# Kernel optimization log

Hardware: AMD Instinct MI355X
Metric: run time of the kernel (lower is better)

The kernel has to match this reference:

```python
import jax, jax.numpy as jnp
import numpy as np

HEADS = 8
DIM_HEAD = 64


def setup_inputs() -> dict:
    key = jax.random.key(0)
    ks = jax.random.split(key, 9)
    b, n, d = 2, 2048, 512
    inner = HEADS * DIM_HEAD  # 512
    s = 0.02
    return {
        "x": jax.random.normal(ks[0], (b, n, d), dtype=jnp.float32),
        "attn_bias": jax.random.normal(ks[1], (1, HEADS, n, n), dtype=jnp.float32),
        "Wq": jax.random.normal(ks[2], (d, inner), dtype=jnp.float32) * s,
        "Wkv": jax.random.normal(ks[3], (d, 2 * inner), dtype=jnp.float32) * s,
        "Wo": jax.random.normal(ks[4], (inner, d), dtype=jnp.float32) * s,
        "bo": jax.random.normal(ks[5], (d,), dtype=jnp.float32) * s,
        "Wg": jax.random.normal(ks[6], (d, inner), dtype=jnp.float32) * s,
        "bg": jnp.ones((inner,), dtype=jnp.float32),
    }


def reference(x, attn_bias, Wq, Wkv, Wo, bo, Wg, bg):
    b, n, d = x.shape
    h, dh = HEADS, DIM_HEAD
    scale = dh ** -0.5
    # projections: [b, n, h*dh] -> [b, h, n, dh]
    q = (x @ Wq).reshape(b, n, h, dh).transpose(0, 2, 1, 3) * scale
    k, v = jnp.split(x @ Wkv, 2, axis=-1)
    k = k.reshape(b, n, h, dh).transpose(0, 2, 1, 3)
    v = v.reshape(b, n, h, dh).transpose(0, 2, 1, 3)
    # scores + additive bias; max-subtract softmax (stable, as in original)
    dots = jnp.einsum('bhid,bhjd->bhij', q, k) + attn_bias
    attn = jax.nn.softmax(dots, axis=-1)
    out = jnp.einsum('bhij,bhjd->bhid', attn, v)
    out = out.transpose(0, 2, 1, 3).reshape(b, n, h * dh)
    # gating sigmoid epilogue
    gates = jax.nn.sigmoid(x @ Wg + bg)
    out = out * gates
    return out @ Wo + bo
```

## Files before the change

kernel.cpp:

```cpp
#include <hip/hip_runtime.h>
#include <hip/hip_bf16.h>

typedef __bf16 bf16_t;
typedef __bf16 bf16x8 __attribute__((ext_vector_type(8)));
typedef __bf16 bf16x4 __attribute__((ext_vector_type(4)));
typedef short short4v __attribute__((ext_vector_type(4)));
typedef float f32x4 __attribute__((ext_vector_type(4)));

static __device__ __forceinline__ bf16_t to_bf16(float f) { return (bf16_t)f; }

static __device__ __forceinline__ f32x4 mfma16x16x16bf16(bf16x4 a, bf16x4 b, f32x4 c) {
#if __has_builtin(__builtin_amdgcn_mfma_f32_16x16x16bf16_1k)
  return __builtin_amdgcn_mfma_f32_16x16x16bf16_1k(
      *reinterpret_cast<short4v*>(&a), *reinterpret_cast<short4v*>(&b), c, 0, 0, 0);
#else
  f32x4 d;
  asm volatile("v_mfma_f32_16x16x16_bf16 %0, %1, %2, %3"
               : "=v"(d) : "v"(a), "v"(b), "v"(c));
  return d;
#endif
}

__global__ void k_convert_x(const float* __restrict__ src, bf16_t* __restrict__ dst, int n8) {
  int i = blockIdx.x * blockDim.x + threadIdx.x;
  if (i >= n8) return;
  const float4* s = reinterpret_cast<const float4*>(src) + (size_t)i * 2;
  float4 a = s[0], b = s[1];
  bf16x8 v;
  v[0]=(bf16_t)a.x; v[1]=(bf16_t)a.y; v[2]=(bf16_t)a.z; v[3]=(bf16_t)a.w;
  v[4]=(bf16_t)b.x; v[5]=(bf16_t)b.y; v[6]=(bf16_t)b.z; v[7]=(bf16_t)b.w;
  reinterpret_cast<bf16x8*>(dst)[i] = v;
}

__global__ void k_transpose_cvt(const float* __restrict__ src, bf16_t* __restrict__ dst, int Nc) {
  __shared__ bf16_t tile[64 * 72];
  const int n0 = blockIdx.x * 64, k0 = blockIdx.y * 64;
  const int t = threadIdx.x;
  #pragma unroll
  for (int it = 0; it < 16; ++it) {
    int c = t + it * 256;
    int kl = c >> 6, nl = c & 63;
    tile[kl * 72 + nl] = to_bf16(src[(size_t)(k0 + kl) * Nc + n0 + nl]);
  }
  __syncthreads();
  #pragma unroll
  for (int it = 0; it < 16; ++it) {
    int c = t + it * 256;
    int nl = c >> 6, kl = c & 63;
    dst[(size_t)(n0 + nl) * 512 + k0 + kl] = tile[kl * 72 + nl];
  }
}

__global__ __launch_bounds__(256) void k_gemm_proj(
    const bf16_t* __restrict__ A,
    const bf16_t* __restrict__ BT,
    const float*  __restrict__ bg,
    bf16_t* __restrict__ qo,
    bf16_t* __restrict__ ko,
    bf16_t* __restrict__ vto,
    float*  __restrict__ go)
{
  __shared__ __align__(16) bf16_t lA[128 * 72];
  __shared__ __align__(16) bf16_t lB[128 * 72];
  const int t = threadIdx.x;
  const int w = t >> 6, lane = t & 63, lr = lane & 15, lg = lane >> 4;
  const int wr = w >> 1, wc = w & 1;
  const int m0 = blockIdx.y * 128, n0 = blockIdx.x * 128;
  f32x4 acc[4][4] = {};
  for (int k0 = 0; k0 < 512; k0 += 64) {
    __syncthreads();
    #pragma unroll
    for (int it = 0; it < 4; ++it) {
      int c = t + it * 256;
      int row = c >> 3, cc = c & 7;
      *reinterpret_cast<bf16x8*>(&lA[row * 72 + cc * 8]) =
          *reinterpret_cast<const bf16x8*>(&A[(size_t)(m0 + row) * 512 + k0 + cc * 8]);
      *reinterpret_cast<bf16x8*>(&lB[row * 72 + cc * 8]) =
          *reinterpret_cast<const bf16x8*>(&BT[(size_t)(n0 + row) * 512 + k0 + cc * 8]);
    }
    __syncthreads();
    #pragma unroll
    for (int kk = 0; kk < 2; ++kk) {
      bf16x8 af[4], bfm[4];
      #pragma unroll
      for (int mf = 0; mf < 4; ++mf)
        af[mf] = *reinterpret_cast<const bf16x8*>(&lA[(wr*64 + mf*16 + lr) * 72 + kk*32 + lg*8]);
      #pragma unroll
      for (int nf = 0; nf < 4; ++nf)
        bfm[nf] = *reinterpret_cast<const bf16x8*>(&lB[(wc*64 + nf*16 + lr) * 72 + kk*32 + lg*8]);
      #pragma unroll
      for (int mf = 0; mf < 4; ++mf)
        #pragma unroll
        for (int nf = 0; nf < 4; ++nf)
          acc[mf][nf] = __builtin_amdgcn_mfma_f32_16x16x32_bf16(af[mf], bfm[nf], acc[mf][nf], 0, 0, 0);
    }
  }
  const int seg = n0 >> 9;
  #pragma unroll
  for (int mf = 0; mf < 4; ++mf) {
    #pragma unroll
    for (int nf = 0; nf < 4; ++nf) {
      #pragma unroll
      for (int r = 0; r < 4; ++r) {
        int rm = m0 + wr*64 + mf*16 + lg*4 + r;
        int cn = n0 + wc*64 + nf*16 + lr;
        float v = acc[mf][nf][r];
        int b = rm >> 11, n = rm & 2047;
        int c = cn & 511;
        if (seg == 0) {
          int h = c >> 6, dh = c & 63;
          qo[((size_t)(b*8 + h) * 2048 + n) * 64 + dh] = to_bf16(v * 0.125f);
        } else if (seg == 1) {
          int h = c >> 6, dh = c & 63;
          ko[((size_t)(b*8 + h) * 2048 + n) * 64 + dh] = to_bf16(v);
        } else if (seg == 2) {
          int h = c >> 6, dh = c & 63;
          vto[((size_t)(b*8 + h) * 64 + dh) * 2048 + n] = to_bf16(v);
        } else {
          float z = v + bg[c];
          go[(size_t)rm * 512 + c] = 1.0f / (1.0f + __expf(-z));
        }
      }
    }
  }
}

#define M_FIX 8.0f
template<int FINAL>
__global__ __launch_bounds__(256, 4) void k_attn(
    const bf16_t* __restrict__ q,
    const bf16_t* __restrict__ kb,
    const bf16_t* __restrict__ vt,
    const float*  __restrict__ bias,
    const float*  __restrict__ gates,
    bf16_t* __restrict__ ao,
    float* __restrict__ pO,
    float* __restrict__ pl)
{
  __shared__ __align__(16) bf16_t lK[64 * 72];
  __shared__ __align__(16) bf16_t lV[64 * 72];
  const int t = threadIdx.x, w = t >> 6, lane = t & 63, lr = lane & 15, lg = lane >> 4;
  const int bh = blockIdx.y, b = bh >> 3, h = bh & 7;
  const int i0 = blockIdx.x * 64, ib = i0 + w * 16;
  const int ntile = 32 / (int)gridDim.z;
  const int sz = blockIdx.z;
  const int jbase = sz * ntile * 64;

  bf16x8 aq[2];
  const bf16_t* qp = q + ((size_t)bh * 2048 + ib + lr) * 64;
  aq[0] = *reinterpret_cast<const bf16x8*>(qp + lg * 8);
  aq[1] = *reinterpret_cast<const bf16x8*>(qp + 32 + lg * 8);

  float l_lane = 0.f;
  f32x4 accO[4] = {};

  const float* bias_p = bias + (size_t)h * 2048 * 2048 + (size_t)(ib + lr) * 2048 + lg * 4;
  const bf16_t* kp = kb + (size_t)bh * 2048 * 64;
  const bf16_t* vp = vt + (size_t)bh * 64 * 2048;

  const int srow = t >> 3, scc = t & 7;
  const int srow1 = (t + 256) >> 3;

  bf16x8 rK0, rK1, rV0, rV1;
  float4 bv4[4];
  {
    const int j0 = jbase;
    rK0 = *reinterpret_cast<const bf16x8*>(&kp[(size_t)(j0 + srow)  * 64 + scc * 8]);
    rK1 = *reinterpret_cast<const bf16x8*>(&kp[(size_t)(j0 + srow1) * 64 + scc * 8]);
    rV0 = *reinterpret_cast<const bf16x8*>(&vp[(size_t)srow  * 2048 + j0 + scc * 8]);
    rV1 = *reinterpret_cast<const bf16x8*>(&vp[(size_t)srow1 * 2048 + j0 + scc * 8]);
    #pragma unroll
    for (int nf = 0; nf < 4; ++nf)
      bv4[nf] = *reinterpret_cast<const float4*>(&bias_p[j0 + nf * 16]);
  }

  for (int jt = 0; jt < ntile; ++jt) {
    const int j1 = jbase + (jt + 1) * 64;
    const bool more = (jt + 1 < ntile);

    __syncthreads();
    *reinterpret_cast<bf16x8*>(&lK[srow  * 72 + scc * 8]) = rK0;
    *reinterpret_cast<bf16x8*>(&lK[srow1 * 72 + scc * 8]) = rK1;
    *reinterpret_cast<bf16x8*>(&lV[srow  * 72 + scc * 8]) = rV0;
    *reinterpret_cast<bf16x8*>(&lV[srow1 * 72 + scc * 8]) = rV1;
    __syncthreads();

    if (more) {
      rK0 = *reinterpret_cast<const bf16x8*>(&kp[(size_t)(j1 + srow)  * 64 + scc * 8]);
      rK1 = *reinterpret_cast<const bf16x8*>(&kp[(size_t)(j1 + srow1) * 64 + scc * 8]);
      rV0 = *reinterpret_cast<const bf16x8*>(&vp[(size_t)srow  * 2048 + j1 + scc * 8]);
      rV1 = *reinterpret_cast<const bf16x8*>(&vp[(size_t)srow1 * 2048 + j1 + scc * 8]);
    }

    f32x4 s[4] = {};
    #pragma unroll
    for (int kk = 0; kk < 2; ++kk) {
      bf16x8 kf[4];
      #pragma unroll
      for (int nf = 0; nf < 4; ++nf)
        kf[nf] = *reinterpret_cast<const bf16x8*>(&lK[(nf*16 + lr) * 72 + kk*32 + lg*8]);
      #pragma unroll
      for (int nf = 0; nf < 4; ++nf)
        s[nf] = __builtin_amdgcn_mfma_f32_16x16x32_bf16(kf[nf], aq[kk], s[nf], 0, 0, 0);
    }

    bf16x4 pa[4];
    #pragma unroll
    for (int nf = 0; nf < 4; ++nf) {
      #pragma unroll
      for (int r = 0; r < 4; ++r) {
        float p = __expf(s[nf][r] + bv4[nf][r] - M_FIX);
        l_lane += p;
        pa[nf][r] = to_bf16(p);
      }
    }
    if (more) {
      #pragma unroll
      for (int nf = 0; nf < 4; ++nf)
        bv4[nf] = *reinterpret_cast<const float4*>(&bias_p[j1 + nf * 16]);
    }

    #pragma unroll
    for (int nf = 0; nf < 4; ++nf) {
      #pragma unroll
      for (int df = 0; df < 4; ++df) {
        bf16x4 vb = *reinterpret_cast<const bf16x4*>(&lV[(df*16 + lr) * 72 + nf*16 + lg*4]);
        accO[df] = mfma16x16x16bf16(pa[nf], vb, accO[df]);
      }
    }
  }

  float rs = l_lane;
  rs += __shfl_xor(rs, 16);
  rs += __shfl_xor(rs, 32);

  if (FINAL) {
    #pragma unroll
    for (int r = 0; r < 4; ++r) {
      float inv = 1.0f / __shfl(rs, lg * 4 + r);
      int ig = ib + lg*4 + r;
      #pragma unroll
      for (int df = 0; df < 4; ++df) {
        int dg = h*64 + df*16 + lr;
        float gate = gates[(size_t)(b*2048 + ig) * 512 + dg];
        ao[(size_t)(b*2048 + ig) * 512 + dg] = to_bf16(accO[df][r] * inv * gate);
      }
    }
  } else {
    float* po = pO + (((size_t)sz * 16 + bh) * 2048) * 64;
    #pragma unroll
    for (int r = 0; r < 4; ++r) {
      int ig = ib + lg*4 + r;
      #pragma unroll
      for (int df = 0; df < 4; ++df)
        po[(size_t)ig * 64 + df*16 + lr] = accO[df][r];
    }
    if (lane < 16) {
      size_t rb = ((size_t)sz * 16 + bh) * 2048 + ib;
      pl[rb + lane] = rs;
    }
  }
}

__global__ __launch_bounds__(256) void k_attn_combine(
    const float* __restrict__ pO, const float* __restrict__ pl,
    const float* __restrict__ gates, bf16_t* __restrict__ ao, int nsplit)
{
  int idx = blockIdx.x * 256 + threadIdx.x;
  int dh = idx & 63, row = (idx >> 6) & 2047, bh = idx >> 17;
  int b = bh >> 3, h = bh & 7;
  const size_t SP_O = (size_t)16 * 2048 * 64, SP_S = (size_t)16 * 2048;
  size_t rb = (size_t)bh * 2048 + row;
  float L = 0.f, O = 0.f;
  for (int s = 0; s < nsplit; ++s) {
    L += pl[s * SP_S + rb];
    O += pO[s * SP_O + rb * 64 + dh];
  }
  float gate = gates[(size_t)(b * 2048 + row) * 512 + h * 64 + dh];
  ao[(size_t)(b * 2048 + row) * 512 + h * 64 + dh] = to_bf16(O / L * gate);
}

__global__ __launch_bounds__(256) void k_gemm_out(
    const bf16_t* __restrict__ A,
    const bf16_t* __restrict__ BT,
    const float*  __restrict__ bo,
    float* __restrict__ out)
{
  __shared__ __align__(16) bf16_t lA[128 * 72];
  __shared__ __align__(16) bf16_t lB[128 * 72];
  const int t = threadIdx.x;
  const int w = t >> 6, lane = t & 63, lr = lane & 15, lg = lane >> 4;
  const int wr = w >> 1, wc = w & 1;
  const int m0 = blockIdx.y * 128, n0 = blockIdx.x * 128;
  f32x4 acc[4][4] = {};
  for (int k0 = 0; k0 < 512; k0 += 64) {
    __syncthreads();
    #pragma unroll
    for (int it = 0; it < 4; ++it) {
      int c = t + it * 256;
      int row = c >> 3, cc = c & 7;
      *reinterpret_cast<bf16x8*>(&lA[row * 72 + cc * 8]) =
          *reinterpret_cast<const bf16x8*>(&A[(size_t)(m0 + row) * 512 + k0 + cc * 8]);
      *reinterpret_cast<bf16x8*>(&lB[row * 72 + cc * 8]) =
          *reinterpret_cast<const bf16x8*>(&BT[(size_t)(n0 + row) * 512 + k0 + cc * 8]);
    }
    __syncthreads();
    #pragma unroll
    for (int kk = 0; kk < 2; ++kk) {
      bf16x8 af[4], bfm[4];
      #pragma unroll
      for (int mf = 0; mf < 4; ++mf)
        af[mf] = *reinterpret_cast<const bf16x8*>(&lA[(wr*64 + mf*16 + lr) * 72 + kk*32 + lg*8]);
      #pragma unroll
      for (int nf = 0; nf < 4; ++nf)
        bfm[nf] = *reinterpret_cast<const bf16x8*>(&lB[(wc*64 + nf*16 + lr) * 72 + kk*32 + lg*8]);
      #pragma unroll
      for (int mf = 0; mf < 4; ++mf)
        #pragma unroll
        for (int nf = 0; nf < 4; ++nf)
          acc[mf][nf] = __builtin_amdgcn_mfma_f32_16x16x32_bf16(af[mf], bfm[nf], acc[mf][nf], 0, 0, 0);
    }
  }
  #pragma unroll
  for (int mf = 0; mf < 4; ++mf) {
    #pragma unroll
    for (int nf = 0; nf < 4; ++nf) {
      #pragma unroll
      for (int r = 0; r < 4; ++r) {
        int rm = m0 + wr*64 + mf*16 + lg*4 + r;
        int cn = n0 + wc*64 + nf*16 + lr;
        out[(size_t)rm * 512 + cn] = acc[mf][nf][r] + bo[cn];
      }
    }
  }
}

extern "C" void kernel_launch(void* const* d_in, const int* in_sizes, int n_in,
                              void* d_out, int out_size, void* d_ws, size_t ws_size,
                              hipStream_t stream) {
  const float* x    = (const float*)d_in[0];
  const float* bias = (const float*)d_in[1];
  const float* Wq   = (const float*)d_in[2];
  const float* Wkv  = (const float*)d_in[3];
  const float* Wo   = (const float*)d_in[4];
  const float* bo   = (const float*)d_in[5];
  const float* Wg   = (const float*)d_in[6];
  const float* bg   = (const float*)d_in[7];
  float* out = (float*)d_out;

  char* ws = (char*)d_ws;
  const size_t MB = 1024 * 1024;
  bf16_t* x_bf  = (bf16_t*)(ws + 0 * MB);
  bf16_t* WcatT = (bf16_t*)(ws + 4 * MB);
  bf16_t* WoT   = (bf16_t*)(ws + 6 * MB);
  bf16_t* q_bf  = (bf16_t*)(ws + 7 * MB);
  bf16_t* k_bf  = (bf16_t*)(ws + 11 * MB);
  bf16_t* vt_bf = (bf16_t*)(ws + 15 * MB);
  float*  g_f32 = (float*) (ws + 19 * MB);
  bf16_t* ao_bf = (bf16_t*)(ws + 27 * MB);
  float*  pO    = (float*) (ws + 31 * MB);
  float*  pl    = (float*) (ws + 47 * MB);

  k_convert_x<<<1024, 256, 0, stream>>>(x, x_bf, 2097152 / 8);
  k_transpose_cvt<<<dim3(8, 8),  256, 0, stream>>>(Wq,  WcatT,               512);
  k_transpose_cvt<<<dim3(16, 8), 256, 0, stream>>>(Wkv, WcatT + 512 * 512,  1024);
  k_transpose_cvt<<<dim3(8, 8),  256, 0, stream>>>(Wg,  WcatT + 1536 * 512,  512);
  k_transpose_cvt<<<dim3(8, 8),  256, 0, stream>>>(Wo,  WoT,                 512);
  k_gemm_proj<<<dim3(16, 32), 256, 0, stream>>>(x_bf, WcatT, bg, q_bf, k_bf, vt_bf, g_f32);

  if (ws_size >= 48 * MB) {
    k_attn<0><<<dim3(32, 16, 2), 256, 0, stream>>>(q_bf, k_bf, vt_bf, bias, nullptr,
                                                   nullptr, pO, pl);
    k_attn_combine<<<8192, 256, 0, stream>>>(pO, pl, g_f32, ao_bf, 2);
  } else {
    k_attn<1><<<dim3(32, 16, 1), 256, 0, stream>>>(q_bf, k_bf, vt_bf, bias, g_f32,
                                                   ao_bf, nullptr, nullptr);
  }
  k_gemm_out<<<dim3(4, 32), 256, 0, stream>>>(ao_bf, WoT, bo, out);
}
```

Baseline: 117.2 us.

## Load K/V fragments directly from global memory, drop LDS staging and barriers

The projection kernel now writes V^T in a tiled layout of 64-key blocks, each stored contiguously as [dh][64 keys]. The attention kernel reads K and V MFMA fragments straight from global memory into registers, so the shared-memory staging, the two barriers per tile and the register double-buffered prefetch are gone. Each wave reloads the same K/V tile on its own, which relies on L1/L2 hits in place of LDS sharing. It also removes explicit software prefetch, so load latency must be hidden by occupancy.

```diff
diff --git a/kernel.cpp b/kernel.cpp
--- a/kernel.cpp
+++ b/kernel.cpp
@@ -115,7 +115,7 @@
           ko[((size_t)(b*8 + h) * 2048 + n) * 64 + dh] = to_bf16(v);
         } else if (seg == 2) {
           int h = c >> 6, dh = c & 63;
-          vto[((size_t)(b*8 + h) * 64 + dh) * 2048 + n] = to_bf16(v);
+          vto[((((size_t)(b*8 + h) * 32 + (n >> 6)) * 64 + dh) * 64) + (n & 63)] = to_bf16(v);
         } else {
           float z = v + bg[c];
           go[(size_t)rm * 512 + c] = 1.0f / (1.0f + __expf(-z));
@@ -137,14 +137,12 @@
     float* __restrict__ pO,
     float* __restrict__ pl)
 {
-  __shared__ __align__(16) bf16_t lK[64 * 72];
-  __shared__ __align__(16) bf16_t lV[64 * 72];
   const int t = threadIdx.x, w = t >> 6, lane = t & 63, lr = lane & 15, lg = lane >> 4;
   const int bh = blockIdx.y, b = bh >> 3, h = bh & 7;
   const int i0 = blockIdx.x * 64, ib = i0 + w * 16;
   const int ntile = 32 / (int)gridDim.z;
   const int sz = blockIdx.z;
-  const int jbase = sz * ntile * 64;
+  const int jt0 = sz * ntile;
 
   bf16x8 aq[2];
   const bf16_t* qp = q + ((size_t)bh * 2048 + ib + lr) * 64;
@@ -154,55 +152,40 @@
   float l_lane = 0.f;
   f32x4 accO[4] = {};
 
-  const float* bias_p = bias + (size_t)h * 2048 * 2048 + (size_t)(ib + lr) * 2048 + lg * 4;
-  const bf16_t* kp = kb + (size_t)bh * 2048 * 64;
-  const bf16_t* vp = vt + (size_t)bh * 64 * 2048;
-
-  const int srow = t >> 3, scc = t & 7;
-  const int srow1 = (t + 256) >> 3;
-
-  bf16x8 rK0, rK1, rV0, rV1;
-  float4 bv4[4];
-  {
-    const int j0 = jbase;
-    rK0 = *reinterpret_cast<const bf16x8*>(&kp[(size_t)(j0 + srow)  * 64 + scc * 8]);
-    rK1 = *reinterpret_cast<const bf16x8*>(&kp[(size_t)(j0 + srow1) * 64 + scc * 8]);
-    rV0 = *reinterpret_cast<const bf16x8*>(&vp[(size_t)srow  * 2048 + j0 + scc * 8]);
-    rV1 = *reinterpret_cast<const bf16x8*>(&vp[(size_t)srow1 * 2048 + j0 + scc * 8]);
+  const bf16_t* kl0 = kb + (size_t)bh * 2048 * 64 + (size_t)(jt0 * 64 + lr) * 64 + lg * 8;
+  const bf16_t* vl0 = vt + ((size_t)bh * 32 + jt0) * 4096 + (size_t)lr * 64 + lg * 4;
+  const float*  bl0 = bias + (size_t)h * 2048 * 2048 + (size_t)(ib + lr) * 2048 + jt0 * 64 + lg * 4;
+
+  for (int jt = 0; jt < ntile; ++jt) {
+    const bf16_t* kT = kl0 + (size_t)jt * 4096;
+    const bf16_t* vT = vl0 + (size_t)jt * 4096;
+    const float*  bT = bl0 + jt * 64;
+
+    bf16x8 kf[2][4];
+    #pragma unroll
+    for (int kk = 0; kk < 2; ++kk)
+      #pragma unroll
+      for (int nf = 0; nf < 4; ++nf)
+        kf[kk][nf] = *reinterpret_cast<const bf16x8*>(&kT[nf * 1024 + kk * 32]);
+
+    float4 bv4[4];
     #pragma unroll
     for (int nf = 0; nf < 4; ++nf)
-      bv4[nf] = *reinterpret_cast<const float4*>(&bias_p[j0 + nf * 16]);
-  }
-
-  for (int jt = 0; jt < ntile; ++jt) {
-    const int j1 = jbase + (jt + 1) * 64;
-    const bool more = (jt + 1 < ntile);
-
-    __syncthreads();
-    *reinterpret_cast<bf16x8*>(&lK[srow  * 72 + scc * 8]) = rK0;
-    *reinterpret_cast<bf16x8*>(&lK[srow1 * 72 + scc * 8]) = rK1;
-    *reinterpret_cast<bf16x8*>(&lV[srow  * 72 + scc * 8]) = rV0;
-    *reinterpret_cast<bf16x8*>(&lV[srow1 * 72 + scc * 8]) = rV1;
-    __syncthreads();
-
-    if (more) {
-      rK0 = *reinterpret_cast<const bf16x8*>(&kp[(size_t)(j1 + srow)  * 64 + scc * 8]);
-      rK1 = *reinterpret_cast<const bf16x8*>(&kp[(size_t)(j1 + srow1) * 64 + scc * 8]);
-      rV0 = *reinterpret_cast<const bf16x8*>(&vp[(size_t)srow  * 2048 + j1 + scc * 8]);
-      rV1 = *reinterpret_cast<const bf16x8*>(&vp[(size_t)srow1 * 2048 + j1 + scc * 8]);
-    }
+      bv4[nf] = *reinterpret_cast<const float4*>(&bT[nf * 16]);
 
     f32x4 s[4] = {};
     #pragma unroll
-    for (int kk = 0; kk < 2; ++kk) {
-      bf16x8 kf[4];
+    for (int kk = 0; kk < 2; ++kk)
       #pragma unroll
       for (int nf = 0; nf < 4; ++nf)
-        kf[nf] = *reinterpret_cast<const bf16x8*>(&lK[(nf*16 + lr) * 72 + kk*32 + lg*8]);
-      #pragma unroll
-      for (int nf = 0; nf < 4; ++nf)
-        s[nf] = __builtin_amdgcn_mfma_f32_16x16x32_bf16(kf[nf], aq[kk], s[nf], 0, 0, 0);
-    }
+        s[nf] = __builtin_amdgcn_mfma_f32_16x16x32_bf16(kf[kk][nf], aq[kk], s[nf], 0, 0, 0);
+
+    bf16x4 vb[4][4];
+    #pragma unroll
+    for (int nf = 0; nf < 4; ++nf)
+      #pragma unroll
+      for (int df = 0; df < 4; ++df)
+        vb[nf][df] = *reinterpret_cast<const bf16x4*>(&vT[df * 1024 + nf * 16]);
 
     bf16x4 pa[4];
     #pragma unroll
@@ -214,20 +197,12 @@
         pa[nf][r] = to_bf16(p);
       }
     }
-    if (more) {
-      #pragma unroll
-      for (int nf = 0; nf < 4; ++nf)
-        bv4[nf] = *reinterpret_cast<const float4*>(&bias_p[j1 + nf * 16]);
-    }
-
-    #pragma unroll
-    for (int nf = 0; nf < 4; ++nf) {
-      #pragma unroll
-      for (int df = 0; df < 4; ++df) {
-        bf16x4 vb = *reinterpret_cast<const bf16x4*>(&lV[(df*16 + lr) * 72 + nf*16 + lg*4]);
-        accO[df] = mfma16x16x16bf16(pa[nf], vb, accO[df]);
-      }
-    }
+
+    #pragma unroll
+    for (int nf = 0; nf < 4; ++nf)
+      #pragma unroll
+      for (int df = 0; df < 4; ++df)
+        accO[df] = mfma16x16x16bf16(pa[nf], vb[nf][df], accO[df]);
   }
 
   float rs = l_lane;
```

Result: slower. 264.7 us (+125.8%).

## Halve attention block size and pre-swizzle V tile in LDS for vector reads

Applied to the files above, without the earlier changes.

The attention kernel now runs 128-thread blocks covering 32 query rows, doubling the grid, and each thread stages four K and V rows per tile. V is stored in LDS in an MFMA-fragment-ordered layout split into two planes, so each lane reads one 16-byte vector per df and feeds four MFMAs. The aim is fewer, wider LDS reads and more blocks for scheduling. The cost is that each K/V tile is loaded from global memory by twice as many blocks, and the strided bf16x4 LDS stores may hit bank conflicts.

```diff
diff --git a/kernel.cpp b/kernel.cpp
--- a/kernel.cpp
+++ b/kernel.cpp
@@ -127,7 +127,7 @@
 
 #define M_FIX 8.0f
 template<int FINAL>
-__global__ __launch_bounds__(256, 4) void k_attn(
+__global__ __launch_bounds__(128, 4) void k_attn(
     const bf16_t* __restrict__ q,
     const bf16_t* __restrict__ kb,
     const bf16_t* __restrict__ vt,
@@ -138,10 +138,10 @@
     float* __restrict__ pl)
 {
   __shared__ __align__(16) bf16_t lK[64 * 72];
-  __shared__ __align__(16) bf16_t lV[64 * 72];
+  __shared__ __align__(16) bf16_t lV[2][2048];
   const int t = threadIdx.x, w = t >> 6, lane = t & 63, lr = lane & 15, lg = lane >> 4;
   const int bh = blockIdx.y, b = bh >> 3, h = bh & 7;
-  const int i0 = blockIdx.x * 64, ib = i0 + w * 16;
+  const int i0 = blockIdx.x * 32, ib = i0 + w * 16;
   const int ntile = 32 / (int)gridDim.z;
   const int sz = blockIdx.z;
   const int jbase = sz * ntile * 64;
@@ -158,17 +158,19 @@
   const bf16_t* kp = kb + (size_t)bh * 2048 * 64;
   const bf16_t* vp = vt + (size_t)bh * 64 * 2048;
 
-  const int srow = t >> 3, scc = t & 7;
-  const int srow1 = (t + 256) >> 3;
-
-  bf16x8 rK0, rK1, rV0, rV1;
+  const int sr = t >> 3, scc = t & 7;
+  const int vplane = scc >> 2, vhalf = (scc >> 1) & 1, lg0 = (scc & 1) * 2;
+
+  bf16x8 rK[4], rV[4];
   float4 bv4[4];
   {
     const int j0 = jbase;
-    rK0 = *reinterpret_cast<const bf16x8*>(&kp[(size_t)(j0 + srow)  * 64 + scc * 8]);
-    rK1 = *reinterpret_cast<const bf16x8*>(&kp[(size_t)(j0 + srow1) * 64 + scc * 8]);
-    rV0 = *reinterpret_cast<const bf16x8*>(&vp[(size_t)srow  * 2048 + j0 + scc * 8]);
-    rV1 = *reinterpret_cast<const bf16x8*>(&vp[(size_t)srow1 * 2048 + j0 + scc * 8]);
+    #pragma unroll
+    for (int rr = 0; rr < 4; ++rr) {
+      int row = sr + rr * 16;
+      rK[rr] = *reinterpret_cast<const bf16x8*>(&kp[(size_t)(j0 + row) * 64 + scc * 8]);
+      rV[rr] = *reinterpret_cast<const bf16x8*>(&vp[(size_t)row * 2048 + j0 + scc * 8]);
+    }
     #pragma unroll
     for (int nf = 0; nf < 4; ++nf)
       bv4[nf] = *reinterpret_cast<const float4*>(&bias_p[j0 + nf * 16]);
@@ -179,17 +181,24 @@
     const bool more = (jt + 1 < ntile);
 
     __syncthreads();
-    *reinterpret_cast<bf16x8*>(&lK[srow  * 72 + scc * 8]) = rK0;
-    *reinterpret_cast<bf16x8*>(&lK[srow1 * 72 + scc * 8]) = rK1;
-    *reinterpret_cast<bf16x8*>(&lV[srow  * 72 + scc * 8]) = rV0;
-    *reinterpret_cast<bf16x8*>(&lV[srow1 * 72 + scc * 8]) = rV1;
+    #pragma unroll
+    for (int rr = 0; rr < 4; ++rr) {
+      int row = sr + rr * 16;
+      *reinterpret_cast<bf16x8*>(&lK[row * 72 + scc * 8]) = rK[rr];
+      *reinterpret_cast<bf16x4*>(&lV[vplane][(rr*64 + lg0*16       + (sr & 15)) * 8 + vhalf*4]) =
+          __builtin_shufflevector(rV[rr], rV[rr], 0, 1, 2, 3);
+      *reinterpret_cast<bf16x4*>(&lV[vplane][(rr*64 + (lg0+1)*16   + (sr & 15)) * 8 + vhalf*4]) =
+          __builtin_shufflevector(rV[rr], rV[rr], 4, 5, 6, 7);
+    }
     __syncthreads();
 
     if (more) {
-      rK0 = *reinterpret_cast<const bf16x8*>(&kp[(size_t)(j1 + srow)  * 64 + scc * 8]);
-      rK1 = *reinterpret_cast<const bf16x8*>(&kp[(size_t)(j1 + srow1) * 64 + scc * 8]);
-      rV0 = *reinterpret_cast<const bf16x8*>(&vp[(size_t)srow  * 2048 + j1 + scc * 8]);
-      rV1 = *reinterpret_cast<const bf16x8*>(&vp[(size_t)srow1 * 2048 + j1 + scc * 8]);
+      #pragma unroll
+      for (int rr = 0; rr < 4; ++rr) {
+        int row = sr + rr * 16;
+        rK[rr] = *reinterpret_cast<const bf16x8*>(&kp[(size_t)(j1 + row) * 64 + scc * 8]);
+        rV[rr] = *reinterpret_cast<const bf16x8*>(&vp[(size_t)row * 2048 + j1 + scc * 8]);
+      }
     }
 
     f32x4 s[4] = {};
@@ -221,12 +230,13 @@
     }
 
     #pragma unroll
-    for (int nf = 0; nf < 4; ++nf) {
-      #pragma unroll
-      for (int df = 0; df < 4; ++df) {
-        bf16x4 vb = *reinterpret_cast<const bf16x4*>(&lV[(df*16 + lr) * 72 + nf*16 + lg*4]);
-        accO[df] = mfma16x16x16bf16(pa[nf], vb, accO[df]);
-      }
+    for (int df = 0; df < 4; ++df) {
+      bf16x8 v01 = *reinterpret_cast<const bf16x8*>(&lV[0][(df*64 + lane) * 8]);
+      bf16x8 v23 = *reinterpret_cast<const bf16x8*>(&lV[1][(df*64 + lane) * 8]);
+      accO[df] = mfma16x16x16bf16(pa[0], __builtin_shufflevector(v01, v01, 0,1,2,3), accO[df]);
+      accO[df] = mfma16x16x16bf16(pa[1], __builtin_shufflevector(v01, v01, 4,5,6,7), accO[df]);
+      accO[df] = mfma16x16x16bf16(pa[2], __builtin_shufflevector(v23, v23, 0,1,2,3), accO[df]);
+      accO[df] = mfma16x16x16bf16(pa[3], __builtin_shufflevector(v23, v23, 4,5,6,7), accO[df]);
     }
   }
 
@@ -369,11 +379,11 @@
   k_gemm_proj<<<dim3(16, 32), 256, 0, stream>>>(x_bf, WcatT, bg, q_bf, k_bf, vt_bf, g_f32);
 
   if (ws_size >= 48 * MB) {
-    k_attn<0><<<dim3(32, 16, 2), 256, 0, stream>>>(q_bf, k_bf, vt_bf, bias, nullptr,
+    k_attn<0><<<dim3(64, 16, 2), 128, 0, stream>>>(q_bf, k_bf, vt_bf, bias, nullptr,
                                                    nullptr, pO, pl);
     k_attn_combine<<<8192, 256, 0, stream>>>(pO, pl, g_f32, ao_bf, 2);
   } else {
-    k_attn<1><<<dim3(32, 16, 1), 256, 0, stream>>>(q_bf, k_bf, vt_bf, bias, g_f32,
+    k_attn<1><<<dim3(64, 16, 1), 128, 0, stream>>>(q_bf, k_bf, vt_bf, bias, g_f32,
                                                    ao_bf, nullptr, nullptr);
   }
   k_gemm_out<<<dim3(4, 32), 256, 0, stream>>>(ao_bf, WoT, bo, out);
```

Measured after the change: 144.6 us. +23.4%, slower.
